# Performance work log

Hardware: AMD Instinct MI355X
Metric: run time of the kernel (lower is better)

Reference implementation:

```python
import jax, jax.numpy as jnp
import numpy as np

N_NODES = 20000
N_EDGES = 320000
N_GRAPHS = 64
IN_FEAT = 64
HIDDEN = 256
GRID = 4
NUM_LAYERS = 4  # -> 3 Fourier message-passing layers
NEG_SLOPE = 0.01  # nn.LeakyReLU default


def setup_inputs() -> dict:
    key = jax.random.key(0)
    ks = jax.random.split(key, 8)
    h = jax.random.normal(ks[0], (N_NODES, IN_FEAT), dtype=jnp.float32)
    src = jax.random.randint(ks[1], (N_EDGES,), 0, N_NODES, dtype=jnp.int32)
    dst = jax.random.randint(ks[2], (N_EDGES,), 0, N_NODES, dtype=jnp.int32)
    graph_ids = jnp.sort(jax.random.randint(ks[3], (N_NODES,), 0, N_GRAPHS, dtype=jnp.int32))
    # KAN_polynomial(in_feat, hidden, degree=grid_feat), init randn/(sqrt(in)*sqrt(deg))
    W_line = jax.random.normal(ks[4], (HIDDEN, IN_FEAT, GRID + 1), dtype=jnp.float32) / (
        np.sqrt(IN_FEAT) * np.sqrt(GRID))
    # 3 NaiveFourierKANLayer coeffs [2, out, in, grid]
    fourier_coeffs = jax.random.normal(ks[5], (NUM_LAYERS - 1, 2, HIDDEN, HIDDEN, GRID),
                                       dtype=jnp.float32) / (np.sqrt(HIDDEN) * np.sqrt(GRID))
    # Readout KAN_polynomial(hidden, 1, degree=1, addbias=True)
    W_out = jax.random.normal(ks[6], (1, HIDDEN, 2), dtype=jnp.float32) / np.sqrt(HIDDEN)
    b_out = jnp.zeros((1, 1), dtype=jnp.float32)
    return {"h": h, "src": src, "dst": dst, "graph_ids": graph_ids,
            "W_line": W_line, "fourier_coeffs": fourier_coeffs,
            "W_out": W_out, "b_out": b_out}


def kan_polynomial(x, coeffs, bias=None):
    # x: [b, in], coeffs: [out, in, deg+1]
    deg = coeffs.shape[-1] - 1
    powers = jnp.stack([x ** i for i in range(deg + 1)], axis=-1)  # [b, in, deg+1]
    y = jnp.einsum('bid,oid->bo', powers, coeffs)
    if bias is not None:
        y = y + bias
    return y


def fourier_kan(x, coeffs):
    # x: [N, in], coeffs: [2, out, in, grid]
    grid = coeffs.shape[-1]
    k = jnp.arange(1, grid + 1, dtype=x.dtype)  # [grid]
    ang = x[:, :, None] * k  # [N, in, grid]
    y = jnp.einsum('nig,oig->no', jnp.cos(ang), coeffs[0])
    y = y + jnp.einsum('nig,oig->no', jnp.sin(ang), coeffs[1])
    return y


def reference(h, src, dst, graph_ids, W_line, fourier_coeffs, W_out, b_out):
    # kan_line
    h = kan_polynomial(h, W_line)  # [N, hidden]
    # message-passing Fourier KAN layers with residual + leaky_relu
    for l in range(NUM_LAYERS - 1):
        agg = jax.ops.segment_sum(h[src], dst, num_segments=N_NODES)  # copy_u + sum
        m = fourier_kan(agg, fourier_coeffs[l])
        h = jax.nn.leaky_relu(m + h, negative_slope=NEG_SLOPE)
    # avg pooling per graph
    sums = jax.ops.segment_sum(h, graph_ids, num_segments=N_GRAPHS)  # [G, hidden]
    counts = jax.ops.segment_sum(jnp.ones((N_NODES,), dtype=h.dtype), graph_ids,
                                 num_segments=N_GRAPHS)
    y = sums / jnp.maximum(counts, 1.0)[:, None]
    # Readout: KAN_polynomial(hidden, 1, degree=1) + sigmoid
    out = jax.nn.sigmoid(kan_polynomial(y, W_out, b_out))  # [G, 1]
    return out
```

## Files before the change

kernel.cpp:

```cpp
#include <hip/hip_runtime.h>
#include <math.h>

#define N_NODES   20000
#define N_PAD2    20096
#define N_EDGES   320000
#define N_GRAPHS  64
#define IN_FEAT   64
#define HIDDEN    256
#define GRID_F    4
#define NLAYERS   3
#define NEG_SLOPE 0.01f

#define KF 2048
#define KL4 256
#define NB_SCAN 79
#define NRG  157
#define NBLK (NRG * 4)
#define NLBLK 1256

typedef _Float16 f16x8 __attribute__((ext_vector_type(8)));
typedef _Float16 f16x2 __attribute__((ext_vector_type(2)));
typedef float    f32x4 __attribute__((ext_vector_type(4)));
typedef unsigned short u16x4 __attribute__((ext_vector_type(4)));

__device__ __forceinline__ unsigned short phase16(float v) {
    float r = v * 0.15915494309189535f;
    r -= floorf(r);
    return (unsigned short)((unsigned)(r * 65536.f + 0.5f) & 0xFFFFu);
}

__global__ void transpose_fourier_f16(const float* __restrict__ fc, _Float16* __restrict__ Bt) {
    int idx = blockIdx.x * 256 + threadIdx.x;
    int kk  = idx & 2047;
    int rest = idx >> 11;
    int o = rest & 255;
    int l = rest >> 8;
    int i = kk >> 3, f = kk & 7, g = f >> 1, t = f & 1;
    Bt[idx] = (_Float16)fc[(((size_t)(l * 2 + t) * HIDDEN + o) * HIDDEN + i) * GRID_F + g];
}

__global__ void transpose_line4(const float* __restrict__ wl, _Float16* __restrict__ Wth,
                                _Float16* __restrict__ Wtl) {
    int idx = blockIdx.x * 256 + threadIdx.x;
    int o = idx >> 8, kk = idx & 255;
    int i = kk >> 2, d = (kk & 3) + 1;
    float wv = wl[(o * IN_FEAT + i) * 5 + d];
    _Float16 h = (_Float16)wv;
    Wth[idx] = h;
    Wtl[idx] = (_Float16)(wv - (float)h);
}

__global__ void line_bias(const float* __restrict__ wl, float* __restrict__ biasv) {
    int o = threadIdx.x;
    float s = 0.f;
    for (int i = 0; i < IN_FEAT; ++i) s += wl[(o * IN_FEAT + i) * 5];
    biasv[o] = s;
}

__global__ void count_deg(const int* __restrict__ dst, int* __restrict__ counts) {
    int e = blockIdx.x * 256 + threadIdx.x;
    if (e < N_EDGES) atomicAdd(&counts[dst[e]], 1);
}

__global__ void block_sums(const int* __restrict__ counts, int* __restrict__ bsum) {
    int i = blockIdx.x * 256 + threadIdx.x;
    int v = (i < N_NODES) ? counts[i] : 0;
    #pragma unroll
    for (int o = 32; o > 0; o >>= 1) v += __shfl_down(v, o, 64);
    __shared__ int ws[4];
    if ((threadIdx.x & 63) == 0) ws[threadIdx.x >> 6] = v;
    __syncthreads();
    if (threadIdx.x == 0) bsum[blockIdx.x] = ws[0] + ws[1] + ws[2] + ws[3];
}

__global__ void scan_mid(const int* __restrict__ bsum, int* __restrict__ bofs,
                         int* __restrict__ row_start) {
    __shared__ int buf[128];
    int t = threadIdx.x;
    int v = (t < NB_SCAN) ? bsum[t] : 0;
    buf[t] = v;
    __syncthreads();
    for (int d = 1; d < 128; d <<= 1) {
        int x = (t >= d) ? buf[t - d] : 0;
        __syncthreads();
        buf[t] += x;
        __syncthreads();
    }
    if (t < NB_SCAN) bofs[t] = buf[t] - v;
    if (t == NB_SCAN - 1) row_start[N_NODES] = buf[t];
}

__global__ void scan_blocks(const int* __restrict__ counts, const int* __restrict__ bofs,
                            int* __restrict__ row_start) {
    int i = blockIdx.x * 256 + threadIdx.x;
    int val = (i < N_NODES) ? counts[i] : 0;
    int lane = threadIdx.x & 63, wid = threadIdx.x >> 6;
    int v = val;
    #pragma unroll
    for (int d = 1; d < 64; d <<= 1) {
        int t = __shfl_up(v, d, 64);
        if (lane >= d) v += t;
    }
    __shared__ int ws[4];
    if (lane == 63) ws[wid] = v;
    __syncthreads();
    int wofs = 0;
    for (int j = 0; j < wid; ++j) wofs += ws[j];
    if (i < N_NODES) row_start[i] = bofs[blockIdx.x] + wofs + v - val;
}

__global__ void fill_csr(const int* __restrict__ src, const int* __restrict__ dst,
                         const int* __restrict__ row_start, int* __restrict__ cursor,
                         int* __restrict__ ssrc) {
    int e = blockIdx.x * 256 + threadIdx.x;
    if (e < N_EDGES) {
        int d = dst[e];
        int pos = row_start[d] + atomicAdd(&cursor[d], 1);
        ssrc[pos] = src[e];
    }
}

__global__ __launch_bounds__(256)
void aggregate(const unsigned short* __restrict__ hq, const int* __restrict__ row_start,
               const int* __restrict__ ssrc, unsigned* __restrict__ cs) {
    const int node = blockIdx.x * 4 + (threadIdx.x >> 6);
    const int lane = threadIdx.x & 63;
    const int b = row_start[node], e = row_start[node + 1];
    u16x4 a0 = {0, 0, 0, 0}, a1 = {0, 0, 0, 0}, a2 = {0, 0, 0, 0}, a3 = {0, 0, 0, 0};
    int j = b;
    for (; j + 3 < e; j += 4) {
        int s0 = ssrc[j], s1 = ssrc[j + 1], s2 = ssrc[j + 2], s3 = ssrc[j + 3];
        a0 += *(const u16x4*)&hq[(size_t)s0 * HIDDEN + lane * 4];
        a1 += *(const u16x4*)&hq[(size_t)s1 * HIDDEN + lane * 4];
        a2 += *(const u16x4*)&hq[(size_t)s2 * HIDDEN + lane * 4];
        a3 += *(const u16x4*)&hq[(size_t)s3 * HIDDEN + lane * 4];
    }
    for (; j < e; ++j) {
        int s0 = ssrc[j];
        a0 += *(const u16x4*)&hq[(size_t)s0 * HIDDEN + lane * 4];
    }
    u16x4 s = (a0 + a1) + (a2 + a3);
    unsigned csv[4];
    #pragma unroll
    for (int k = 0; k < 4; ++k) {
        float r = (float)s[k] * (1.f / 65536.f);
        _Float16 ch = (_Float16)__builtin_amdgcn_cosf(r);
        _Float16 sh = (_Float16)__builtin_amdgcn_sinf(r);
        union { f16x2 z; unsigned u; } p;
        p.z = (f16x2){ch, sh};
        csv[k] = p.u;
    }
    *(uint4*)&cs[(size_t)node * HIDDEN + lane * 4] = make_uint4(csv[0], csv[1], csv[2], csv[3]);
}

__device__ __forceinline__ void makepow(float xa, float xb, f16x8& hi, f16x8& lo) {
    float p0 = xa, p1 = xa * xa;
    float p2 = p1 * xa, p3 = p1 * p1;
    float q0 = xb, q1 = xb * xb;
    float q2 = q1 * xb, q3 = q1 * q1;
    float pp[8] = {p0, p1, p2, p3, q0, q1, q2, q3};
    #pragma unroll
    for (int j = 0; j < 8; ++j) {
        _Float16 h = (_Float16)pp[j];
        hi[j] = h;
        lo[j] = (_Float16)(pp[j] - (float)h);
    }
}

__global__ __launch_bounds__(256)
void kan_line_mfma(const float* __restrict__ x, const _Float16* __restrict__ Wth,
                   const _Float16* __restrict__ Wtl, const float* __restrict__ biasv,
                   float* __restrict__ out, unsigned short* __restrict__ hqo) {
    __shared__ float    As[64][64];
    __shared__ _Float16 Bsh[64][136];
    __shared__ _Float16 Bsl[64][136];

    const int t = threadIdx.x;
    const int w = t >> 6, l = t & 63, ln = l & 15, quad = l >> 4;
    const int wr = w >> 1, wc = w & 1;

    const int g   = blockIdx.x;
    const int bid = (g & 7) * 157 + (g >> 3);
    const int Mbase = (bid >> 2) * 64;
    const int col0  = (bid & 3) * 64;

    #pragma unroll
    for (int r = 0; r < 4; ++r) {
        int idx = r * 256 + t;
        int row = idx >> 4, p = idx & 15;
        int grow = Mbase + row;
        if (grow > N_NODES - 1) grow = N_NODES - 1;
        f32x4 v = *(const f32x4*)&x[(size_t)grow * IN_FEAT + p * 4];
        *(f32x4*)&As[row][(p * 4) ^ ((row & 7) << 2)] = v;
    }
    const _Float16* WthB = Wth + (size_t)col0 * KL4;
    const _Float16* WtlB = Wtl + (size_t)col0 * KL4;
    #pragma unroll
    for (int r = 0; r < 4; ++r) {
        int idx = r * 256 + t;
        int c = idx >> 4, p = idx & 15;
        *(f16x8*)&Bsh[c][p * 8] = *(const f16x8*)&WthB[(size_t)c * KL4 + p * 8];
        *(f16x8*)&Bsl[c][p * 8] = *(const f16x8*)&WtlB[(size_t)c * KL4 + p * 8];
    }
    f16x8 pbh[4], pbl[4];
    #pragma unroll
    for (int r = 0; r < 4; ++r) {
        int idx = r * 256 + t;
        int c = idx >> 4, p = idx & 15;
        pbh[r] = *(const f16x8*)&WthB[(size_t)c * KL4 + 128 + p * 8];
        pbl[r] = *(const f16x8*)&WtlB[(size_t)c * KL4 + 128 + p * 8];
    }
    __syncthreads();

    f32x4 acc[2][2];
    #pragma unroll
    for (int rt = 0; rt < 2; ++rt)
        #pragma unroll
        for (int ct = 0; ct < 2; ++ct)
            acc[rt][ct] = (f32x4){0.f, 0.f, 0.f, 0.f};

    const int lr0 = wr * 32 + ln;
    const int xsw = (lr0 & 7) << 2;

    #pragma unroll
    for (int half = 0; half < 2; ++half) {
        #pragma unroll
        for (int kcl = 0; kcl < 4; ++kcl) {
            const int kc = half * 4 + kcl;
            const int f0 = kc * 8 + quad * 2;
            float x00 = As[lr0     ][f0 ^ xsw];
            float x01 = As[lr0     ][(f0 + 1) ^ xsw];
            float x10 = As[lr0 + 16][f0 ^ xsw];
            float x11 = As[lr0 + 16][(f0 + 1) ^ xsw];
            f16x8 ah0, al0, ah1, al1;
            makepow(x00, x01, ah0, al0);
            makepow(x10, x11, ah1, al1);
            #pragma unroll
            for (int ct = 0; ct < 2; ++ct) {
                const int bc = wc * 32 + ct * 16 + ln;
                f16x8 bh = *(const f16x8*)&Bsh[bc][kcl * 32 + quad * 8];
                f16x8 bl = *(const f16x8*)&Bsl[bc][kcl * 32 + quad * 8];
                acc[0][ct] = __builtin_amdgcn_mfma_f32_16x16x32_f16(ah0, bh, acc[0][ct], 0, 0, 0);
                acc[0][ct] = __builtin_amdgcn_mfma_f32_16x16x32_f16(al0, bh, acc[0][ct], 0, 0, 0);
                acc[0][ct] = __builtin_amdgcn_mfma_f32_16x16x32_f16(ah0, bl, acc[0][ct], 0, 0, 0);
                acc[1][ct] = __builtin_amdgcn_mfma_f32_16x16x32_f16(ah1, bh, acc[1][ct], 0, 0, 0);
                acc[1][ct] = __builtin_amdgcn_mfma_f32_16x16x32_f16(al1, bh, acc[1][ct], 0, 0, 0);
                acc[1][ct] = __builtin_amdgcn_mfma_f32_16x16x32_f16(ah1, bl, acc[1][ct], 0, 0, 0);
            }
        }
        if (half == 0) {
            __syncthreads();
            #pragma unroll
            for (int r = 0; r < 4; ++r) {
                int idx = r * 256 + t;
                int c = idx >> 4, p = idx & 15;
                *(f16x8*)&Bsh[c][p * 8] = pbh[r];
                *(f16x8*)&Bsl[c][p * 8] = pbl[r];
            }
            __syncthreads();
        }
    }

    #pragma unroll
    for (int rt = 0; rt < 2; ++rt) {
        const int row0 = Mbase + wr * 32 + rt * 16 + quad * 4;
        #pragma unroll
        for (int ct = 0; ct < 2; ++ct) {
            const int col = col0 + wc * 32 + ct * 16 + ln;
            const float bv = biasv[col];
            #pragma unroll
            for (int r = 0; r < 4; ++r) {
                const int row = row0 + r;
                if (row < N_NODES) {
                    float vv = acc[rt][ct][r] + bv;
                    out[(size_t)row * HIDDEN + col] = vv;
                    hqo[(size_t)row * HIDDEN + col] = phase16(vv);
                }
            }
        }
    }
}

__device__ __forceinline__ f16x8 expand4(unsigned csu) {
    union { unsigned u; f16x2 z; } w; w.u = csu;
    f16x2 z1 = w.z;
    f16x2 cc = {z1[0], z1[0]};
    f16x2 ms = {(_Float16)(-z1[1]), z1[1]};
    f16x2 z2 = z1 * cc + (f16x2){z1[1], z1[0]} * ms;
    f16x2 z3 = z2 * cc + (f16x2){z2[1], z2[0]} * ms;
    f16x2 z4 = z3 * cc + (f16x2){z3[1], z3[0]} * ms;
    union { f16x8 v; f16x2 p[4]; } u;
    u.p[0] = z1; u.p[1] = z2; u.p[2] = z3; u.p[3] = z4;
    return u.v;
}

__global__ __launch_bounds__(512)
void fourier_mfma(const unsigned* __restrict__ cs, float* hio,
                  const _Float16* __restrict__ Bt, unsigned short* __restrict__ hqo) {
    __shared__ _Float16 Bs[2][64][140];
    __shared__ unsigned As[2][128][17];

    const int t    = threadIdx.x;
    const int w    = t >> 6;
    const int l    = t & 63;
    const int ln   = l & 15;
    const int quad = l >> 4;

    const int g   = blockIdx.x;
    const int xcd = g & 7, ii = g >> 3;
    const int bid = (xcd < 4 ? xcd * 79 : 316 + (xcd - 4) * 78) + ii;
    const int Mbase = (bid >> 2) * 128;
    const int col0  = (bid & 3) * 64;

    const int sc = t >> 4, sp = t & 15;
    const int sr = t >> 2, sq = t & 3;
    const _Float16* bgA = Bt + (size_t)(col0 + sc) * KF + sp * 8;
    const _Float16* bgB = bgA + (size_t)32 * KF;
    const unsigned* ag  = cs + (size_t)(Mbase + sr) * HIDDEN + sq * 4;

    f32x4 acc[4];
    #pragma unroll
    for (int ct = 0; ct < 4; ++ct) acc[ct] = (f32x4){0.f, 0.f, 0.f, 0.f};

    f16x8 sbA, sbB;
    uint4 sa;

    sbA = *(const f16x8*)(bgA);
    sbB = *(const f16x8*)(bgB);
    sa  = *(const uint4*)(ag);
    *(f16x8*)&Bs[0][sc     ][sp * 8] = sbA;
    *(f16x8*)&Bs[0][sc + 32][sp * 8] = sbB;
    As[0][sr][sq * 4 + 0] = sa.x;
    As[0][sr][sq * 4 + 1] = sa.y;
    As[0][sr][sq * 4 + 2] = sa.z;
    As[0][sr][sq * 4 + 3] = sa.w;
    __syncthreads();

    const int lr0 = w * 16 + ln;

    for (int kg = 0; kg < 16; ++kg) {
        const int b = kg & 1;
        if (kg < 15) {
            sbA = *(const f16x8*)(bgA + (kg + 1) * 128);
            sbB = *(const f16x8*)(bgB + (kg + 1) * 128);
            sa  = *(const uint4*)(ag + (kg + 1) * 16);
        }
        #pragma unroll
        for (int kc = 0; kc < 4; ++kc) {
            unsigned cv = As[b][lr0][kc * 4 + quad];
            f16x8 b0 = *(const f16x8*)&Bs[b][ln     ][kc * 32 + quad * 8];
            f16x8 b1 = *(const f16x8*)&Bs[b][ln + 16][kc * 32 + quad * 8];
            f16x8 b2 = *(const f16x8*)&Bs[b][ln + 32][kc * 32 + quad * 8];
            f16x8 b3 = *(const f16x8*)&Bs[b][ln + 48][kc * 32 + quad * 8];
            f16x8 a = expand4(cv);
            acc[0] = __builtin_amdgcn_mfma_f32_16x16x32_f16(a, b0, acc[0], 0, 0, 0);
            acc[1] = __builtin_amdgcn_mfma_f32_16x16x32_f16(a, b1, acc[1], 0, 0, 0);
            acc[2] = __builtin_amdgcn_mfma_f32_16x16x32_f16(a, b2, acc[2], 0, 0, 0);
            acc[3] = __builtin_amdgcn_mfma_f32_16x16x32_f16(a, b3, acc[3], 0, 0, 0);
        }
        if (kg < 15) {
            const int nb = b ^ 1;
            *(f16x8*)&Bs[nb][sc     ][sp * 8] = sbA;
            *(f16x8*)&Bs[nb][sc + 32][sp * 8] = sbB;
            As[nb][sr][sq * 4 + 0] = sa.x;
            As[nb][sr][sq * 4 + 1] = sa.y;
            As[nb][sr][sq * 4 + 2] = sa.z;
            As[nb][sr][sq * 4 + 3] = sa.w;
        }
        __syncthreads();
    }

    const int row0 = Mbase + w * 16 + quad * 4;
    #pragma unroll
    for (int ct = 0; ct < 4; ++ct) {
        const int col = col0 + ct * 16 + ln;
        #pragma unroll
        for (int r = 0; r < 4; ++r) {
            const int row = row0 + r;
            if (row < N_NODES) {
                float v = acc[ct][r] + hio[(size_t)row * HIDDEN + col];
                v = v > 0.f ? v : NEG_SLOPE * v;
                hio[(size_t)row * HIDDEN + col] = v;
                hqo[(size_t)row * HIDDEN + col] = phase16(v);
            }
        }
    }
}

__global__ void graph_bounds(const int* __restrict__ gid, int* __restrict__ gstart) {
    int g = threadIdx.x;
    if (g < N_GRAPHS) {
        int lo = 0, hi = N_NODES;
        while (lo < hi) { int mid = (lo + hi) >> 1; if (gid[mid] < g) lo = mid + 1; else hi = mid; }
        gstart[g] = lo;
    } else if (g == N_GRAPHS) {
        gstart[g] = N_NODES;
    }
}

__global__ __launch_bounds__(256)
void pool_seg(const float* __restrict__ h, const int* __restrict__ gid,
              float* __restrict__ pooled) {
    const int c = threadIdx.x;
    const int s = blockIdx.x * 128;
    const int e = min(s + 128, N_NODES);
    float acc = 0.f;
    int g = gid[s];
    for (int n = s; n < e; ++n) {
        int gn = gid[n];
        if (gn != g) {
            atomicAdd(&pooled[g * HIDDEN + c], acc);
            acc = 0.f;
            g = gn;
        }
        acc += h[(size_t)n * HIDDEN + c];
    }
    atomicAdd(&pooled[g * HIDDEN + c], acc);
}

__global__ void readout(const float* __restrict__ pooled, const int* __restrict__ gstart,
                        const float* __restrict__ wout, const float* __restrict__ bout,
                        float* __restrict__ out) {
    int g = blockIdx.x, t = threadIdx.x;
    float cnt = fmaxf((float)(gstart[g + 1] - gstart[g]), 1.f);
    float y = pooled[g * HIDDEN + t] / cnt;
    float term = wout[t * 2 + 0] + wout[t * 2 + 1] * y;
    #pragma unroll
    for (int o = 32; o > 0; o >>= 1) term += __shfl_down(term, o, 64);
    __shared__ float wsum[4];
    if ((t & 63) == 0) wsum[t >> 6] = term;
    __syncthreads();
    if (t == 0) {
        float s = wsum[0] + wsum[1] + wsum[2] + wsum[3] + bout[0];
        out[g] = 1.f / (1.f + expf(-s));
    }
}

extern "C" void kernel_launch(void* const* d_in, const int* in_sizes, int n_in,
                              void* d_out, int out_size, void* d_ws, size_t ws_size,
                              hipStream_t stream) {
    const float* h_in  = (const float*)d_in[0];
    const int*   src   = (const int*)d_in[1];
    const int*   dst   = (const int*)d_in[2];
    const int*   gid   = (const int*)d_in[3];
    const float* wline = (const float*)d_in[4];
    const float* fcoef = (const float*)d_in[5];
    const float* wout  = (const float*)d_in[6];
    const float* bout  = (const float*)d_in[7];
    float* out = (float*)d_out;

    char* ws = (char*)d_ws;
    size_t off = 0;
    auto alloc = [&](size_t bytes) {
        size_t o = off;
        off += (bytes + 255) & ~size_t(255);
        return o;
    };
    float*          hbuf      = (float*)(ws + alloc((size_t)N_PAD2 * HIDDEN * 4));
    unsigned short* hqbuf     = (unsigned short*)(ws + alloc((size_t)N_PAD2 * HIDDEN * 2));
    unsigned*       csbuf     = (unsigned*)(ws + alloc((size_t)N_PAD2 * HIDDEN * 4));
    _Float16*       BtF16     = (_Float16*)(ws + alloc((size_t)NLAYERS * KF * HIDDEN * 2));
    _Float16*       Wth       = (_Float16*)(ws + alloc((size_t)HIDDEN * KL4 * 2));
    _Float16*       Wtl       = (_Float16*)(ws + alloc((size_t)HIDDEN * KL4 * 2));
    float*          biasv     = (float*)(ws + alloc((size_t)HIDDEN * 4));
    int*            row_start = (int*)(ws + alloc((size_t)(N_NODES + 1) * 4));
    int*            counts    = (int*)(ws + alloc((size_t)N_NODES * 4));
    int*            cursor    = (int*)(ws + alloc((size_t)N_NODES * 4));
    int*            ssrc      = (int*)(ws + alloc((size_t)N_EDGES * 4));
    int*            bsum      = (int*)(ws + alloc((size_t)128 * 4));
    int*            bofs      = (int*)(ws + alloc((size_t)128 * 4));
    int*            gstart    = (int*)(ws + alloc((size_t)(N_GRAPHS + 1) * 4));
    float*          pooled    = (float*)(ws + alloc((size_t)N_GRAPHS * HIDDEN * 4));

    hipMemsetAsync(counts, 0, (size_t)N_NODES * 4, stream);
    hipMemsetAsync(cursor, 0, (size_t)N_NODES * 4, stream);
    hipMemsetAsync(pooled, 0, (size_t)N_GRAPHS * HIDDEN * 4, stream);
    hipMemsetAsync(csbuf + (size_t)N_NODES * HIDDEN, 0,
                   (size_t)(N_PAD2 - N_NODES) * HIDDEN * 4, stream);

    transpose_fourier_f16<<<6144, 256, 0, stream>>>(fcoef, BtF16);
    transpose_line4<<<256, 256, 0, stream>>>(wline, Wth, Wtl);
    line_bias<<<1, 256, 0, stream>>>(wline, biasv);
    count_deg<<<(N_EDGES + 255) / 256, 256, 0, stream>>>(dst, counts);
    block_sums<<<NB_SCAN, 256, 0, stream>>>(counts, bsum);
    scan_mid<<<1, 128, 0, stream>>>(bsum, bofs, row_start);
    scan_blocks<<<NB_SCAN, 256, 0, stream>>>(counts, bofs, row_start);
    fill_csr<<<(N_EDGES + 255) / 256, 256, 0, stream>>>(src, dst, row_start, cursor, ssrc);
    graph_bounds<<<1, 128, 0, stream>>>(gid, gstart);

    kan_line_mfma<<<NLBLK, 256, 0, stream>>>(h_in, Wth, Wtl, biasv, hbuf, hqbuf);

    for (int l = 0; l < NLAYERS; ++l) {
        aggregate<<<N_NODES / 4, 256, 0, stream>>>(hqbuf, row_start, ssrc, csbuf);
        fourier_mfma<<<NBLK, 512, 0, stream>>>(csbuf, hbuf,
                                               BtF16 + (size_t)l * KF * HIDDEN, hqbuf);
    }

    pool_seg<<<(N_NODES + 127) / 128, 256, 0, stream>>>(hbuf, gid, pooled);
    readout<<<N_GRAPHS, 256, 0, stream>>>(pooled, gstart, wout, bout, out);
}
```

Measured before the change: 396.7 us.

## Switch Fourier GEMM to 32x32x16 MFMA with 64x64 warp tiles, 128 threads

The Fourier layer GEMM drops from 8 waves per block, each computing a 16x64 tile with 16x16x32 MFMAs, to 2 waves per block, each computing a 64x64 tile with 32x32x16 MFMAs. Each wave now reuses every A and B fragment read from LDS across two MFMAs, which cuts LDS traffic and repeated expand4 trig-recurrence work per MFMA. With fewer threads, each thread stages more global loads (8 B and 4 A vectors) per k-step. The costs are higher register pressure from 64 accumulator floats per lane, less latency hiding per block, and a scattered epilogue store pattern.

```diff
diff --git a/kernel.cpp b/kernel.cpp
--- a/kernel.cpp
+++ b/kernel.cpp
@@ -21,6 +21,7 @@
 typedef _Float16 f16x8 __attribute__((ext_vector_type(8)));
 typedef _Float16 f16x2 __attribute__((ext_vector_type(2)));
 typedef float    f32x4 __attribute__((ext_vector_type(4)));
+typedef float    f32x16 __attribute__((ext_vector_type(16)));
 typedef unsigned short u16x4 __attribute__((ext_vector_type(4)));
 
 __device__ __forceinline__ unsigned short phase16(float v) {
@@ -294,17 +295,17 @@
     return u.v;
 }
 
-__global__ __launch_bounds__(512)
+__global__ __launch_bounds__(128)
 void fourier_mfma(const unsigned* __restrict__ cs, float* hio,
                   const _Float16* __restrict__ Bt, unsigned short* __restrict__ hqo) {
     __shared__ _Float16 Bs[2][64][140];
     __shared__ unsigned As[2][128][17];
 
-    const int t    = threadIdx.x;
-    const int w    = t >> 6;
-    const int l    = t & 63;
-    const int ln   = l & 15;
-    const int quad = l >> 4;
+    const int t  = threadIdx.x;
+    const int w  = t >> 6;
+    const int l  = t & 63;
+    const int m  = l & 31;
+    const int hi = l >> 5;
 
     const int g   = blockIdx.x;
     const int xcd = g & 7, ii = g >> 3;
@@ -314,74 +315,90 @@
 
     const int sc = t >> 4, sp = t & 15;
     const int sr = t >> 2, sq = t & 3;
-    const _Float16* bgA = Bt + (size_t)(col0 + sc) * KF + sp * 8;
-    const _Float16* bgB = bgA + (size_t)32 * KF;
-    const unsigned* ag  = cs + (size_t)(Mbase + sr) * HIDDEN + sq * 4;
-
-    f32x4 acc[4];
-    #pragma unroll
-    for (int ct = 0; ct < 4; ++ct) acc[ct] = (f32x4){0.f, 0.f, 0.f, 0.f};
-
-    f16x8 sbA, sbB;
-    uint4 sa;
-
-    sbA = *(const f16x8*)(bgA);
-    sbB = *(const f16x8*)(bgB);
-    sa  = *(const uint4*)(ag);
-    *(f16x8*)&Bs[0][sc     ][sp * 8] = sbA;
-    *(f16x8*)&Bs[0][sc + 32][sp * 8] = sbB;
-    As[0][sr][sq * 4 + 0] = sa.x;
-    As[0][sr][sq * 4 + 1] = sa.y;
-    As[0][sr][sq * 4 + 2] = sa.z;
-    As[0][sr][sq * 4 + 3] = sa.w;
+    const _Float16* bg = Bt + (size_t)(col0 + sc) * KF + sp * 8;
+    const unsigned* ag = cs + (size_t)(Mbase + sr) * HIDDEN + sq * 4;
+
+    f32x16 acc[2][2];
+    #pragma unroll
+    for (int rg = 0; rg < 2; ++rg)
+        #pragma unroll
+        for (int cg = 0; cg < 2; ++cg)
+            #pragma unroll
+            for (int r = 0; r < 16; ++r) acc[rg][cg][r] = 0.f;
+
+    f16x8 sb[8];
+    uint4 sa[4];
+
+    #pragma unroll
+    for (int i = 0; i < 8; ++i) sb[i] = *(const f16x8*)(bg + (size_t)(8 * i) * KF);
+    #pragma unroll
+    for (int i = 0; i < 4; ++i) sa[i] = *(const uint4*)(ag + (size_t)(32 * i) * HIDDEN);
+    #pragma unroll
+    for (int i = 0; i < 8; ++i) *(f16x8*)&Bs[0][sc + 8 * i][sp * 8] = sb[i];
+    #pragma unroll
+    for (int i = 0; i < 4; ++i) {
+        As[0][sr + 32 * i][sq * 4 + 0] = sa[i].x;
+        As[0][sr + 32 * i][sq * 4 + 1] = sa[i].y;
+        As[0][sr + 32 * i][sq * 4 + 2] = sa[i].z;
+        As[0][sr + 32 * i][sq * 4 + 3] = sa[i].w;
+    }
     __syncthreads();
 
-    const int lr0 = w * 16 + ln;
+    const int ar0 = w * 64 + m;
 
     for (int kg = 0; kg < 16; ++kg) {
         const int b = kg & 1;
         if (kg < 15) {
-            sbA = *(const f16x8*)(bgA + (kg + 1) * 128);
-            sbB = *(const f16x8*)(bgB + (kg + 1) * 128);
-            sa  = *(const uint4*)(ag + (kg + 1) * 16);
+            #pragma unroll
+            for (int i = 0; i < 8; ++i)
+                sb[i] = *(const f16x8*)(bg + (size_t)(8 * i) * KF + (kg + 1) * 128);
+            #pragma unroll
+            for (int i = 0; i < 4; ++i)
+                sa[i] = *(const uint4*)(ag + (size_t)(32 * i) * HIDDEN + (kg + 1) * 16);
         }
         #pragma unroll
-        for (int kc = 0; kc < 4; ++kc) {
-            unsigned cv = As[b][lr0][kc * 4 + quad];
-            f16x8 b0 = *(const f16x8*)&Bs[b][ln     ][kc * 32 + quad * 8];
-            f16x8 b1 = *(const f16x8*)&Bs[b][ln + 16][kc * 32 + quad * 8];
-            f16x8 b2 = *(const f16x8*)&Bs[b][ln + 32][kc * 32 + quad * 8];
-            f16x8 b3 = *(const f16x8*)&Bs[b][ln + 48][kc * 32 + quad * 8];
-            f16x8 a = expand4(cv);
-            acc[0] = __builtin_amdgcn_mfma_f32_16x16x32_f16(a, b0, acc[0], 0, 0, 0);
-            acc[1] = __builtin_amdgcn_mfma_f32_16x16x32_f16(a, b1, acc[1], 0, 0, 0);
-            acc[2] = __builtin_amdgcn_mfma_f32_16x16x32_f16(a, b2, acc[2], 0, 0, 0);
-            acc[3] = __builtin_amdgcn_mfma_f32_16x16x32_f16(a, b3, acc[3], 0, 0, 0);
+        for (int step = 0; step < 8; ++step) {
+            unsigned cv0 = As[b][ar0     ][step * 2 + hi];
+            unsigned cv1 = As[b][ar0 + 32][step * 2 + hi];
+            f16x8 b0 = *(const f16x8*)&Bs[b][m     ][step * 16 + hi * 8];
+            f16x8 b1 = *(const f16x8*)&Bs[b][m + 32][step * 16 + hi * 8];
+            f16x8 a0 = expand4(cv0);
+            f16x8 a1 = expand4(cv1);
+            acc[0][0] = __builtin_amdgcn_mfma_f32_32x32x16_f16(a0, b0, acc[0][0], 0, 0, 0);
+            acc[0][1] = __builtin_amdgcn_mfma_f32_32x32x16_f16(a0, b1, acc[0][1], 0, 0, 0);
+            acc[1][0] = __builtin_amdgcn_mfma_f32_32x32x16_f16(a1, b0, acc[1][0], 0, 0, 0);
+            acc[1][1] = __builtin_amdgcn_mfma_f32_32x32x16_f16(a1, b1, acc[1][1], 0, 0, 0);
         }
         if (kg < 15) {
             const int nb = b ^ 1;
-            *(f16x8*)&Bs[nb][sc     ][sp * 8] = sbA;
-            *(f16x8*)&Bs[nb][sc + 32][sp * 8] = sbB;
-            As[nb][sr][sq * 4 + 0] = sa.x;
-            As[nb][sr][sq * 4 + 1] = sa.y;
-            As[nb][sr][sq * 4 + 2] = sa.z;
-            As[nb][sr][sq * 4 + 3] = sa.w;
+            #pragma unroll
+            for (int i = 0; i < 8; ++i) *(f16x8*)&Bs[nb][sc + 8 * i][sp * 8] = sb[i];
+            #pragma unroll
+            for (int i = 0; i < 4; ++i) {
+                As[nb][sr + 32 * i][sq * 4 + 0] = sa[i].x;
+                As[nb][sr + 32 * i][sq * 4 + 1] = sa[i].y;
+                As[nb][sr + 32 * i][sq * 4 + 2] = sa[i].z;
+                As[nb][sr + 32 * i][sq * 4 + 3] = sa[i].w;
+            }
         }
         __syncthreads();
     }
 
-    const int row0 = Mbase + w * 16 + quad * 4;
-    #pragma unroll
-    for (int ct = 0; ct < 4; ++ct) {
-        const int col = col0 + ct * 16 + ln;
+    #pragma unroll
+    for (int rg = 0; rg < 2; ++rg) {
+        const int rbase = Mbase + w * 64 + rg * 32 + 4 * hi;
         #pragma unroll
-        for (int r = 0; r < 4; ++r) {
-            const int row = row0 + r;
-            if (row < N_NODES) {
-                float v = acc[ct][r] + hio[(size_t)row * HIDDEN + col];
-                v = v > 0.f ? v : NEG_SLOPE * v;
-                hio[(size_t)row * HIDDEN + col] = v;
-                hqo[(size_t)row * HIDDEN + col] = phase16(v);
+        for (int cg = 0; cg < 2; ++cg) {
+            const int col = col0 + cg * 32 + m;
+            #pragma unroll
+            for (int r = 0; r < 16; ++r) {
+                const int row = rbase + (r & 3) + 8 * (r >> 2);
+                if (row < N_NODES) {
+                    float v = acc[rg][cg][r] + hio[(size_t)row * HIDDEN + col];
+                    v = v > 0.f ? v : NEG_SLOPE * v;
+                    hio[(size_t)row * HIDDEN + col] = v;
+                    hqo[(size_t)row * HIDDEN + col] = phase16(v);
+                }
             }
         }
     }
@@ -492,7 +509,7 @@
 
     for (int l = 0; l < NLAYERS; ++l) {
         aggregate<<<N_NODES / 4, 256, 0, stream>>>(hqbuf, row_start, ssrc, csbuf);
-        fourier_mfma<<<NBLK, 512, 0, stream>>>(csbuf, hbuf,
+        fourier_mfma<<<NBLK, 128, 0, stream>>>(csbuf, hbuf,
                                                BtF16 + (size_t)l * KF * HIDDEN, hqbuf);
     }
 
```

Result: slower. 422.8 us (+6.6%).
